# Kernel optimization log

Hardware: AMD Instinct MI355X
Metric: run time of the kernel (lower is better)

Reference implementation:

```python
import jax, jax.numpy as jnp
import numpy as np

N = 4096
FEAT = 64


def _pairwise_dist(x):
    # x: [N, F] -> symmetric [N, N] Euclidean distance matrix, zero diagonal
    sq = jnp.sum(x * x, axis=-1)
    d2 = sq[:, None] + sq[None, :] - 2.0 * (x @ x.T)
    d = jnp.sqrt(jnp.maximum(d2, 0.0))
    return d * (1.0 - jnp.eye(x.shape[0], dtype=x.dtype))


def setup_inputs() -> dict:
    key = jax.random.key(0)
    k1, k2 = jax.random.split(key)
    x1 = jax.random.normal(k1, (N, FEAT), dtype=jnp.float32)
    x2 = jax.random.normal(k2, (N, FEAT), dtype=jnp.float32)
    return {"d1": _pairwise_dist(x1), "d2": _pairwise_dist(x2)}


def _mst_edges(d):
    # Prim's algorithm, O(N^2). For a distance matrix with generic (distinct)
    # entries the MST is unique and its N-1 edges are exactly the 0-dim
    # persistence pairs returned by the union-find PersistentHomologyCalculation.
    n = d.shape[0]
    INF = jnp.asarray(jnp.finfo(d.dtype).max, d.dtype)
    in_tree = jnp.zeros((n,), dtype=bool).at[0].set(True)
    min_dist = d[0]                       # best edge weight into the tree per node
    parent = jnp.zeros((n,), dtype=jnp.int32)  # tree endpoint of that best edge

    def step(carry, _):
        in_tree, min_dist, parent = carry
        masked = jnp.where(in_tree, INF, min_dist)
        j = jnp.argmin(masked).astype(jnp.int32)
        edge = jnp.stack([parent[j], j])  # (tree node, new node)
        in_tree = in_tree.at[j].set(True)
        dj = d[j]
        upd = (dj < min_dist) & (~in_tree)
        min_dist = jnp.where(upd, dj, min_dist)
        parent = jnp.where(upd, j, parent)
        return (in_tree, min_dist, parent), edge

    _, edges = jax.lax.scan(step, (in_tree, min_dist, parent), None, length=n - 1)
    return edges  # [N-1, 2] int32; d is symmetric so pair order is irrelevant


def reference(d1, d2):
    # Pairings are computed on detached CPU copies in the original -> no grad
    p1 = _mst_edges(jax.lax.stop_gradient(d1))
    p2 = jax.lax.stop_gradient(_mst_edges(jax.lax.stop_gradient(d2)))
    sig1 = d1[p1[:, 0], p1[:, 1]]
    sig2 = d2[p2[:, 0], p2[:, 1]]
    # match_edges == 'symmetric'
    sig1_2 = d2[p1[:, 0], p1[:, 1]]
    sig2_1 = d1[p2[:, 0], p2[:, 1]]
    return jnp.sum((sig1 - sig1_2) ** 2) + jnp.sum((sig2 - sig2_1) ** 2)
```

## Files before the change

### kernel.cpp

```cpp
#include <hip/hip_runtime.h>
#include <stdint.h>


#define N        4096
#define NROUNDS  12

typedef unsigned long long u64;
typedef uint32_t u32;

#define INFK (~0ull)

struct Ws {
    u64 best[2][N];
    u32 comp[2][N];
    u32 edges[2][N];
    u32 ncomp[2];
    u32 pad[14];
    u64 bm[2][N * 64];
};

__device__ __forceinline__ u64 umin64(u64 a, u64 b) { return a < b ? a : b; }

__device__ __forceinline__ u64 shfl_down_u64(u64 x, int off) {
    u32 lo = (u32)x, hi = (u32)(x >> 32);
    lo = (u32)__shfl_down((int)lo, off, 64);
    hi = (u32)__shfl_down((int)hi, off, 64);
    return ((u64)hi << 32) | lo;
}
__device__ __forceinline__ u64 shfl_xor_u64(u64 x, int off) {
    u32 lo = (u32)x, hi = (u32)(x >> 32);
    lo = (u32)__shfl_xor((int)lo, off, 64);
    hi = (u32)__shfl_xor((int)hi, off, 64);
    return ((u64)hi << 32) | lo;
}

__global__ void init_k(Ws* __restrict__ ws) {
    int i = blockIdx.x * blockDim.x + threadIdx.x;
    if (i < N) {
        ws->best[0][i] = INFK; ws->best[1][i] = INFK;
        ws->comp[0][i] = (u32)i; ws->comp[1][i] = (u32)i;
        u32 diag = ((u32)i << 12) | (u32)i;
        ws->edges[0][i] = diag; ws->edges[1][i] = diag;
        if (i < 2) ws->ncomp[i] = (u32)N;
    }
}

__launch_bounds__(256, 8)
__global__ void scanA_k(const float* __restrict__ d1, const float* __restrict__ d2,
                        Ws* __restrict__ ws) {
    const int m = blockIdx.x >> 10;
    const int wave = threadIdx.x >> 6, lane = threadIdx.x & 63;
    const int v = ((blockIdx.x & 1023) << 2) + wave;
    const float4* __restrict__ row4 = (const float4*)((m ? d2 : d1) + (size_t)v * N);
    u64* __restrict__ bmrow = ws->bm[m] + (size_t)v * 64;

    __shared__ u64 bs[4][64];

    const u32 uv = (u32)v;
    u64 rowmin = INFK;

    #pragma unroll
    for (int i = 0; i < 16; ++i) {
        const int c = lane + 64 * i;
        float4 w = row4[c];
        const u32 c0 = (u32)(4 * c);
        u64 k0 = (c0 + 0 == uv) ? INFK : ((((u64)__float_as_uint(w.x)) << 12) | (c0 + 0));
        u64 k1 = (c0 + 1 == uv) ? INFK : ((((u64)__float_as_uint(w.y)) << 12) | (c0 + 1));
        u64 k2 = (c0 + 2 == uv) ? INFK : ((((u64)__float_as_uint(w.z)) << 12) | (c0 + 2));
        u64 k3 = (c0 + 3 == uv) ? INFK : ((((u64)__float_as_uint(w.w)) << 12) | (c0 + 3));
        u64 kk = umin64(umin64(k0, k1), umin64(k2, k3));
        #pragma unroll
        for (int off = 1; off <= 8; off <<= 1)
            kk = umin64(kk, shfl_xor_u64(kk, off));
        if ((lane & 15) == 0) bs[wave][4 * i + (lane >> 4)] = kk;
        rowmin = umin64(rowmin, kk);
    }
    rowmin = umin64(rowmin, shfl_xor_u64(rowmin, 16));
    rowmin = umin64(rowmin, shfl_xor_u64(rowmin, 32));

    __syncthreads();
    bmrow[lane] = bs[wave][lane];

    if (lane == 0) {
        u32 wb = (u32)(rowmin >> 12);
        u32 u  = (u32)rowmin & 0xFFFu;
        u32 lo = min(uv, u), hi = max(uv, u);
        ws->best[m][v] = ((u64)wb << 24) | ((u64)lo << 12) | (u64)hi;
    }
}

__launch_bounds__(256, 8)
__global__ void scan2_k(const float* __restrict__ d1, const float* __restrict__ d2,
                        Ws* __restrict__ ws) {
    const int m = blockIdx.x >> 10;
    if (ws->ncomp[m] <= 1u) return;
    const int wave = threadIdx.x >> 6, lane = threadIdx.x & 63;
    const int v = ((blockIdx.x & 1023) << 2) + wave;

    const float* __restrict__ dm = m ? d2 : d1;
    const u32*   __restrict__ cm = ws->comp[m];
    u64* __restrict__ bmrow = ws->bm[m] + (size_t)v * 64;

    const u32 cv = cm[v];
    u64 key = bmrow[lane];
    bool cross = false;
    if (key != INFK) cross = (cm[(u32)key & 0xFFFu] != cv);

    u64 kb = cross ? key : INFK;
    #pragma unroll
    for (int off = 1; off <= 32; off <<= 1)
        kb = umin64(kb, shfl_xor_u64(kb, off));

    const bool need = (!cross) && (key < kb);
    u64 nm = INFK;
    if (need) {
        const float4* __restrict__ row4 = (const float4*)(dm + (size_t)v * N);
        const uint4*  __restrict__ c4   = (const uint4*)cm;
        #pragma unroll
        for (int j = 0; j < 16; ++j) {
            float4 w = row4[lane * 16 + j];
            uint4 cu = c4[lane * 16 + j];
            u32 c0 = (u32)(4 * (lane * 16 + j));
            if (cu.x != cv) nm = umin64(nm, (((u64)__float_as_uint(w.x)) << 12) | (c0 + 0));
            if (cu.y != cv) nm = umin64(nm, (((u64)__float_as_uint(w.y)) << 12) | (c0 + 1));
            if (cu.z != cv) nm = umin64(nm, (((u64)__float_as_uint(w.z)) << 12) | (c0 + 2));
            if (cu.w != cv) nm = umin64(nm, (((u64)__float_as_uint(w.w)) << 12) | (c0 + 3));
        }
        bmrow[lane] = nm;
    }
    u64 kb2 = need ? nm : INFK;
    #pragma unroll
    for (int off = 1; off <= 32; off <<= 1)
        kb2 = umin64(kb2, shfl_xor_u64(kb2, off));

    u64 fin = umin64(kb, kb2);
    if (lane == 0 && fin != INFK) {
        u32 wb = (u32)(fin >> 12);
        u32 u  = (u32)fin & 0xFFFu;
        u32 lo = min((u32)v, u), hi = max((u32)v, u);
        u64 g  = ((u64)wb << 24) | ((u64)lo << 12) | (u64)hi;
        if (g < ws->best[m][cv])
            atomicMin(&ws->best[m][cv], g);
    }
}

__launch_bounds__(256, 8)
__global__ void scanF_k(const float* __restrict__ d1, const float* __restrict__ d2,
                        Ws* __restrict__ ws, int first) {
    const int m = blockIdx.x >> 10;
    if (ws->ncomp[m] <= 1u) return;
    const int wave = threadIdx.x >> 6, lane = threadIdx.x & 63;
    const int v = ((blockIdx.x & 1023) << 2) + wave;
    const float* __restrict__ dm = m ? d2 : d1;
    const u32*   __restrict__ cm = ws->comp[m];
    const float4* __restrict__ row4 = (const float4*)(dm + (size_t)v * N);
    const uint4*  __restrict__ c4   = (const uint4*)cm;
    const u32 cv = first ? (u32)v : cm[v];
    float wmin = __int_as_float(0x7F800000);
    u32 colmin = 0u;
    #pragma unroll
    for (int bb = 0; bb < 4; ++bb) {
        float4 w[4]; uint4 cu[4];
        #pragma unroll
        for (int i = 0; i < 4; ++i) {
            const int c = lane + 64 * (bb * 4 + i);
            w[i] = row4[c];
            if (!first) cu[i] = c4[c];
        }
        #pragma unroll
        for (int i = 0; i < 4; ++i) {
            const u32 c0 = (u32)(4 * (lane + 64 * (bb * 4 + i)));
            if (first) {
                const u32 uv = (u32)v;
                if (c0+0 != uv && w[i].x < wmin) { wmin = w[i].x; colmin = c0+0; }
                if (c0+1 != uv && w[i].y < wmin) { wmin = w[i].y; colmin = c0+1; }
                if (c0+2 != uv && w[i].z < wmin) { wmin = w[i].z; colmin = c0+2; }
                if (c0+3 != uv && w[i].w < wmin) { wmin = w[i].w; colmin = c0+3; }
            } else {
                if (cu[i].x != cv && w[i].x < wmin) { wmin = w[i].x; colmin = c0+0; }
                if (cu[i].y != cv && w[i].y < wmin) { wmin = w[i].y; colmin = c0+1; }
                if (cu[i].z != cv && w[i].z < wmin) { wmin = w[i].z; colmin = c0+2; }
                if (cu[i].w != cv && w[i].w < wmin) { wmin = w[i].w; colmin = c0+3; }
            }
        }
    }
    u64 kmin = ((u64)__float_as_uint(wmin) << 32) | (u64)colmin;
    #pragma unroll
    for (int off = 32; off >= 1; off >>= 1)
        kmin = umin64(kmin, shfl_down_u64(kmin, off));
    if (lane == 0) {
        u32 wb = (u32)(kmin >> 32);
        u32 u  = (u32)kmin & 0xFFFu;
        u32 lo = min((u32)v, u), hi = max((u32)v, u);
        u64 g  = ((u64)wb << 24) | ((u64)lo << 12) | (u64)hi;
        if (first) ws->best[m][v] = g;
        else if (g < ws->best[m][cv]) atomicMin(&ws->best[m][cv], g);
    }
}

__launch_bounds__(1024, 1)
__global__ void hook_k(Ws* __restrict__ ws) {
    const int m = blockIdx.x;
    const int tid = threadIdx.x;
    if (ws->ncomp[m] <= 1u) return;

    u32* __restrict__ gcomp = ws->comp[m];
    u64* __restrict__ best  = ws->best[m];

    __shared__ u32 compL[N];
    __shared__ u32 nxtA[N];
    __shared__ u32 nxtB[N];
    __shared__ u32 red[16];

    {
        uint4* dst = (uint4*)compL;
        const uint4* src = (const uint4*)gcomp;
        if (tid < N / 4) dst[tid] = src[tid];
    }
    __syncthreads();

    bool isroot[4];
    u64  bkey[4];

    #pragma unroll
    for (int k = 0; k < 4; ++k) {
        int i = tid + k * 1024;
        u32 x = (u32)i;
        bool r = (compL[i] == (u32)i);
        isroot[k] = r;
        u64 g = 0;
        if (r) {
            g = best[i];
            u32 lo = (u32)(g >> 12) & 0xFFFu;
            u32 hi = (u32)g & 0xFFFu;
            u32 cl = compL[lo], ch = compL[hi];
            x = (cl == (u32)i) ? ch : cl;
        }
        bkey[k] = g;
        nxtA[i] = x;
    }
    __syncthreads();

    #pragma unroll
    for (int k = 0; k < 4; ++k) {
        int i = tid + k * 1024;
        u32 nn = (u32)i;
        if (isroot[k]) {
            u32 o = nxtA[i];
            bool mutual = (nxtA[o] == (u32)i);
            nn = (mutual && ((u32)i < o)) ? (u32)i : o;
            if (nn != (u32)i)
                ws->edges[m][i] = (u32)(bkey[k] & 0xFFFFFFu);
        }
        nxtB[i] = nn;
    }
    __syncthreads();

    for (int s = 0; s < 12; ++s) {
        #pragma unroll
        for (int k = 0; k < 4; ++k) {
            int i = tid + k * 1024;
            nxtB[i] = nxtB[nxtB[i]];
        }
        __syncthreads();
    }

    u32 cnt = 0;
    #pragma unroll
    for (int k = 0; k < 4; ++k) {
        int i = tid + k * 1024;
        if (isroot[k] && nxtB[i] == (u32)i) cnt++;
    }
    #pragma unroll
    for (int off = 32; off >= 1; off >>= 1) cnt += (u32)__shfl_down((int)cnt, off, 64);
    const int lane = tid & 63, wave = tid >> 6;
    if (lane == 0) red[wave] = cnt;
    __syncthreads();

    #pragma unroll
    for (int k = 0; k < 4; ++k) {
        int i = tid + k * 1024;
        gcomp[i] = nxtB[compL[i]];
        if (isroot[k]) best[i] = INFK;
    }
    if (tid == 0) {
        u32 t = 0;
        #pragma unroll
        for (int w = 0; w < 16; ++w) t += red[w];
        ws->ncomp[m] = t;
    }
}

__launch_bounds__(256, 1)
__global__ void epi_k(const float* __restrict__ d1, const float* __restrict__ d2,
                      Ws* __restrict__ ws, float* __restrict__ out) {
    const int m = blockIdx.x, tid = threadIdx.x;
    float acc = 0.f;
    for (int i = tid; i < N; i += 256) {
        u32 pk = ws->edges[m][i];
        u32 lo = (pk >> 12) & 0xFFFu, hi = pk & 0xFFFu;
        size_t off = (size_t)lo * N + hi;
        float df = d1[off] - d2[off];
        acc += df * df;
    }
    #pragma unroll
    for (int off = 32; off >= 1; off >>= 1) acc += __shfl_down(acc, off, 64);
    __shared__ float part[4];
    const int lane = tid & 63, wave = tid >> 6;
    if (lane == 0) part[wave] = acc;
    __syncthreads();
    if (tid == 0) atomicAdd(out, part[0] + part[1] + part[2] + part[3]);
}

extern "C" void kernel_launch(void* const* d_in, const int* in_sizes, int n_in,
                              void* d_out, int out_size, void* d_ws, size_t ws_size,
                              hipStream_t stream) {
    (void)in_sizes; (void)n_in; (void)out_size;
    const float* d1 = (const float*)d_in[0];
    const float* d2 = (const float*)d_in[1];
    float* out = (float*)d_out;
    Ws* ws = (Ws*)d_ws;
    const bool big = (ws_size >= sizeof(Ws));

    hipMemsetAsync(d_out, 0, sizeof(float), stream);
    init_k<<<dim3(16), dim3(256), 0, stream>>>(ws);
    for (int r = 0; r < NROUNDS; ++r) {
        if (big) {
            if (r == 0) scanA_k<<<dim3(2048), dim3(256), 0, stream>>>(d1, d2, ws);
            else        scan2_k<<<dim3(2048), dim3(256), 0, stream>>>(d1, d2, ws);
        } else {
            scanF_k<<<dim3(2048), dim3(256), 0, stream>>>(d1, d2, ws, r == 0 ? 1 : 0);
        }
        hook_k<<<dim3(2), dim3(1024), 0, stream>>>(ws);
    }
    epi_k<<<dim3(2), dim3(256), 0, stream>>>(d1, d2, ws, out);
}
```

Measured before the change: 281.0 us.

## Use per-lane strided column buckets to cut shuffles and coalesce rescans

Each lane in scanA now keeps a running minimum over its own strided set of columns and writes it as its bucket. This replaces the per-16-lane shuffle reductions, the shared-memory staging and the __syncthreads. scan2 recomputes buckets with the same strided, coalesced float4 indexing, where it used to read contiguous 64-column chunks per lane, which gave uncoalesced loads. scanF is also reduced to a single packed 64-bit key minimum with an xor-butterfly, instead of separate float and index tracking. The risk is that bucket semantics change across kernels, so scanA and scan2 must stay consistent; the strided buckets may also filter rescans less well.

```diff
diff --git a/kernel.cpp b/kernel.cpp
--- a/kernel.cpp
+++ b/kernel.cpp
@@ -54,32 +54,30 @@
     const float4* __restrict__ row4 = (const float4*)((m ? d2 : d1) + (size_t)v * N);
     u64* __restrict__ bmrow = ws->bm[m] + (size_t)v * 64;
 
-    __shared__ u64 bs[4][64];
-
     const u32 uv = (u32)v;
-    u64 rowmin = INFK;
-
-    #pragma unroll
-    for (int i = 0; i < 16; ++i) {
-        const int c = lane + 64 * i;
+    u64 bmin = INFK;
+
+    #pragma unroll
+    for (int j = 0; j < 16; ++j) {
+        const int c = lane + 64 * j;
         float4 w = row4[c];
         const u32 c0 = (u32)(4 * c);
-        u64 k0 = (c0 + 0 == uv) ? INFK : ((((u64)__float_as_uint(w.x)) << 12) | (c0 + 0));
-        u64 k1 = (c0 + 1 == uv) ? INFK : ((((u64)__float_as_uint(w.y)) << 12) | (c0 + 1));
-        u64 k2 = (c0 + 2 == uv) ? INFK : ((((u64)__float_as_uint(w.z)) << 12) | (c0 + 2));
-        u64 k3 = (c0 + 3 == uv) ? INFK : ((((u64)__float_as_uint(w.w)) << 12) | (c0 + 3));
-        u64 kk = umin64(umin64(k0, k1), umin64(k2, k3));
-        #pragma unroll
-        for (int off = 1; off <= 8; off <<= 1)
-            kk = umin64(kk, shfl_xor_u64(kk, off));
-        if ((lane & 15) == 0) bs[wave][4 * i + (lane >> 4)] = kk;
-        rowmin = umin64(rowmin, kk);
-    }
-    rowmin = umin64(rowmin, shfl_xor_u64(rowmin, 16));
-    rowmin = umin64(rowmin, shfl_xor_u64(rowmin, 32));
-
-    __syncthreads();
-    bmrow[lane] = bs[wave][lane];
+        u64 k0 = (((u64)__float_as_uint(w.x)) << 12) | (c0 + 0);
+        u64 k1 = (((u64)__float_as_uint(w.y)) << 12) | (c0 + 1);
+        u64 k2 = (((u64)__float_as_uint(w.z)) << 12) | (c0 + 2);
+        u64 k3 = (((u64)__float_as_uint(w.w)) << 12) | (c0 + 3);
+        if (c0 + 0 != uv) bmin = umin64(bmin, k0);
+        if (c0 + 1 != uv) bmin = umin64(bmin, k1);
+        if (c0 + 2 != uv) bmin = umin64(bmin, k2);
+        if (c0 + 3 != uv) bmin = umin64(bmin, k3);
+    }
+
+    bmrow[lane] = bmin;
+
+    u64 rowmin = bmin;
+    #pragma unroll
+    for (int off = 1; off <= 32; off <<= 1)
+        rowmin = umin64(rowmin, shfl_xor_u64(rowmin, off));
 
     if (lane == 0) {
         u32 wb = (u32)(rowmin >> 12);
@@ -118,9 +116,10 @@
         const uint4*  __restrict__ c4   = (const uint4*)cm;
         #pragma unroll
         for (int j = 0; j < 16; ++j) {
-            float4 w = row4[lane * 16 + j];
-            uint4 cu = c4[lane * 16 + j];
-            u32 c0 = (u32)(4 * (lane * 16 + j));
+            const int c = lane + 64 * j;
+            float4 w = row4[c];
+            uint4 cu = c4[c];
+            u32 c0 = (u32)(4 * c);
             if (cu.x != cv) nm = umin64(nm, (((u64)__float_as_uint(w.x)) << 12) | (c0 + 0));
             if (cu.y != cv) nm = umin64(nm, (((u64)__float_as_uint(w.y)) << 12) | (c0 + 1));
             if (cu.z != cv) nm = umin64(nm, (((u64)__float_as_uint(w.z)) << 12) | (c0 + 2));
@@ -156,40 +155,31 @@
     const float4* __restrict__ row4 = (const float4*)(dm + (size_t)v * N);
     const uint4*  __restrict__ c4   = (const uint4*)cm;
     const u32 cv = first ? (u32)v : cm[v];
-    float wmin = __int_as_float(0x7F800000);
-    u32 colmin = 0u;
-    #pragma unroll
-    for (int bb = 0; bb < 4; ++bb) {
-        float4 w[4]; uint4 cu[4];
-        #pragma unroll
-        for (int i = 0; i < 4; ++i) {
-            const int c = lane + 64 * (bb * 4 + i);
-            w[i] = row4[c];
-            if (!first) cu[i] = c4[c];
-        }
-        #pragma unroll
-        for (int i = 0; i < 4; ++i) {
-            const u32 c0 = (u32)(4 * (lane + 64 * (bb * 4 + i)));
-            if (first) {
-                const u32 uv = (u32)v;
-                if (c0+0 != uv && w[i].x < wmin) { wmin = w[i].x; colmin = c0+0; }
-                if (c0+1 != uv && w[i].y < wmin) { wmin = w[i].y; colmin = c0+1; }
-                if (c0+2 != uv && w[i].z < wmin) { wmin = w[i].z; colmin = c0+2; }
-                if (c0+3 != uv && w[i].w < wmin) { wmin = w[i].w; colmin = c0+3; }
-            } else {
-                if (cu[i].x != cv && w[i].x < wmin) { wmin = w[i].x; colmin = c0+0; }
-                if (cu[i].y != cv && w[i].y < wmin) { wmin = w[i].y; colmin = c0+1; }
-                if (cu[i].z != cv && w[i].z < wmin) { wmin = w[i].z; colmin = c0+2; }
-                if (cu[i].w != cv && w[i].w < wmin) { wmin = w[i].w; colmin = c0+3; }
-            }
-        }
-    }
-    u64 kmin = ((u64)__float_as_uint(wmin) << 32) | (u64)colmin;
-    #pragma unroll
-    for (int off = 32; off >= 1; off >>= 1)
-        kmin = umin64(kmin, shfl_down_u64(kmin, off));
-    if (lane == 0) {
-        u32 wb = (u32)(kmin >> 32);
+    u64 kmin = INFK;
+    #pragma unroll
+    for (int j = 0; j < 16; ++j) {
+        const int c = lane + 64 * j;
+        float4 w = row4[c];
+        uint4 cu;
+        if (!first) cu = c4[c];
+        const u32 c0 = (u32)(4 * c);
+        bool x0, x1, x2, x3;
+        if (first) {
+            const u32 uvv = (u32)v;
+            x0 = (c0+0 != uvv); x1 = (c0+1 != uvv); x2 = (c0+2 != uvv); x3 = (c0+3 != uvv);
+        } else {
+            x0 = (cu.x != cv); x1 = (cu.y != cv); x2 = (cu.z != cv); x3 = (cu.w != cv);
+        }
+        if (x0) kmin = umin64(kmin, (((u64)__float_as_uint(w.x)) << 12) | (c0 + 0));
+        if (x1) kmin = umin64(kmin, (((u64)__float_as_uint(w.y)) << 12) | (c0 + 1));
+        if (x2) kmin = umin64(kmin, (((u64)__float_as_uint(w.z)) << 12) | (c0 + 2));
+        if (x3) kmin = umin64(kmin, (((u64)__float_as_uint(w.w)) << 12) | (c0 + 3));
+    }
+    #pragma unroll
+    for (int off = 1; off <= 32; off <<= 1)
+        kmin = umin64(kmin, shfl_xor_u64(kmin, off));
+    if (lane == 0 && kmin != INFK) {
+        u32 wb = (u32)(kmin >> 12);
         u32 u  = (u32)kmin & 0xFFFu;
         u32 lo = min((u32)v, u), hi = max((u32)v, u);
         u64 g  = ((u64)wb << 24) | ((u64)lo << 12) | (u64)hi;
```

Result: no change. 281.2 us (+0.1%).
